# Optimization experiments

Hardware: AMD Instinct MI355X
Metric: run time of the kernel (lower is better)

## Reference

```python
import jax, jax.numpy as jnp
import numpy as np

TEMPERATURE = 0.07
N, D, NUM_CLASSES = 8192, 1024, 128


def setup_inputs() -> dict:
    key = jax.random.key(0)
    k1, k2 = jax.random.split(key)
    embeddings = jax.random.normal(k1, (N, D), dtype=jnp.float32)
    labels = jax.random.randint(k2, (N,), 0, NUM_CLASSES, dtype=jnp.int64)
    return {"embeddings": embeddings, "labels": labels}


def reference(embeddings, labels):
    # L2-normalize rows (eps matches F.normalize default clamp of 1e-12 on the norm)
    norm = jnp.maximum(jnp.linalg.norm(embeddings, axis=-1, keepdims=True), 1e-12)
    emb = embeddings / norm
    # [N, N] similarity scaled by temperature
    sim = jnp.matmul(emb, emb.T) / TEMPERATURE
    # positive mask: same label, diagonal zeroed
    pos_mask = (labels[:, None] == labels[None, :]).astype(sim.dtype)
    pos_mask = pos_mask * (1.0 - jnp.eye(sim.shape[0], dtype=sim.dtype))
    exp_sim = jnp.exp(sim)
    sum_exp = exp_sim.sum(axis=1)              # [N]
    pos_sum = (exp_sim * pos_mask).sum(axis=1)  # [N]
    loss = -jnp.log(pos_sum / sum_exp)
    return loss.mean()
```

## Files before the change

### kernel.cpp

```cpp
#include <hip/hip_runtime.h>
#include <hip/hip_bf16.h>
#include <math.h>

#define N 8192
#define D 1024
#define BM 256
#define BK 64
#define NTIL 32
#define NBLK 528
#define ITERS 8

typedef __bf16 bf16_t;
typedef bf16_t bf16x4 __attribute__((ext_vector_type(4)));
typedef bf16_t bf16x8 __attribute__((ext_vector_type(8)));
typedef float f32x4 __attribute__((ext_vector_type(4)));

__global__ __launch_bounds__(256) void norm_cast(const float* __restrict__ in,
                                                 bf16_t* __restrict__ out) {
    const int row = blockIdx.x;
    const int tid = threadIdx.x;
    const float4 v = ((const float4*)(in + (size_t)row * D))[tid];
    float ss = v.x * v.x + v.y * v.y + v.z * v.z + v.w * v.w;
    #pragma unroll
    for (int off = 32; off >= 1; off >>= 1) ss += __shfl_xor(ss, off, 64);
    __shared__ float red[4];
    const int wave = tid >> 6, lane = tid & 63;
    if (lane == 0) red[wave] = ss;
    __syncthreads();
    const float tot = red[0] + red[1] + red[2] + red[3];
    const float scale = 1.0f / fmaxf(sqrtf(tot), 1e-12f);
    bf16x4 o;
    o[0] = (bf16_t)(v.x * scale);
    o[1] = (bf16_t)(v.y * scale);
    o[2] = (bf16_t)(v.z * scale);
    o[3] = (bf16_t)(v.w * scale);
    ((bf16x4*)(out + (size_t)row * D))[tid] = o;
}

__global__ __launch_bounds__(512, 2) void gemm_fused(const bf16_t* __restrict__ E,
                                                     const int* __restrict__ labels,
                                                     float* __restrict__ sumExp,
                                                     float* __restrict__ posSum) {
    __shared__ bf16_t As[2][2][128 * 64];
    __shared__ bf16_t Bs[2][2][128 * 64];

    const int b0 = blockIdx.x;
    const int b  = (b0 & 7) * (NBLK / 8) + (b0 >> 3);

    int ti = (int)((sqrtf(8.0f * (float)b + 1.0f) - 1.0f) * 0.5f);
    while ((ti + 1) * (ti + 2) / 2 <= b) ++ti;
    while (ti * (ti + 1) / 2 > b) --ti;
    const int tj = b - ti * (ti + 1) / 2;
    const bool isDiag = (ti == tj);

    const int tid  = threadIdx.x;
    const int wave = tid >> 6;
    const int lane = tid & 63;
    const int lr   = lane & 15;
    const int q    = lane >> 4;
    const int wm   = wave >> 2;
    const int wn   = wave & 3;
    const int rowStart = ti * BM;
    const int colStart = tj * BM;

    f32x4 acc[8][4];
    #pragma unroll
    for (int m = 0; m < 8; ++m)
        #pragma unroll
        for (int n = 0; n < 4; ++n) acc[m][n] = {0.f, 0.f, 0.f, 0.f};

    const int r0  = tid >> 3;
    const int lu0 = (tid & 7) ^ (r0 & 7);
    const char* gA = (const char*)(E + (size_t)rowStart * D) + (size_t)r0 * (D * 2) + lu0 * 16;
    const char* gB = (const char*)(E + (size_t)colStart * D) + (size_t)r0 * (D * 2) + lu0 * 16;

    #define STAGE_A(buf, h, kb) do {                                                     \
        const char* g0_ = gA + (size_t)(h) * (128 * 2048) + (kb);                        \
        char* l0_ = (char*)&As[buf][h][0] + wave * 1024;                                 \
        __builtin_amdgcn_global_load_lds((const __attribute__((address_space(1))) void*)g0_, \
            (__attribute__((address_space(3))) void*)l0_, 16, 0, 0);                     \
        __builtin_amdgcn_global_load_lds(                                                \
            (const __attribute__((address_space(1))) void*)(g0_ + 64 * 2048),            \
            (__attribute__((address_space(3))) void*)(l0_ + 8192), 16, 0, 0);            \
    } while (0)
    #define STAGE_B(buf, h, kb) do {                                                     \
        const char* g0_ = gB + (size_t)(h) * (128 * 2048) + (kb);                        \
        char* l0_ = (char*)&Bs[buf][h][0] + wave * 1024;                                 \
        __builtin_amdgcn_global_load_lds((const __attribute__((address_space(1))) void*)g0_, \
            (__attribute__((address_space(3))) void*)l0_, 16, 0, 0);                     \
        __builtin_amdgcn_global_load_lds(                                                \
            (const __attribute__((address_space(1))) void*)(g0_ + 64 * 2048),            \
            (__attribute__((address_space(3))) void*)(l0_ + 8192), 16, 0, 0);            \
    } while (0)

    const int su0 = ((0 + q) ^ (lane & 7)) * 16;
    const int su1 = ((4 + q) ^ (lane & 7)) * 16;
    const char* rA0 = (const char*)&As[0][wm][0] + lr * 128;
    const char* rA1 = (const char*)&As[1][wm][0] + lr * 128;
    const char* rB0 = (const char*)&Bs[0][wn >> 1][0] + (wn & 1) * 8192 + lr * 128;
    const char* rB1 = (const char*)&Bs[1][wn >> 1][0] + (wn & 1) * 8192 + lr * 128;

    #define LD_A4(DST, RBASE, MOFFB, SU) do {                                            \
        _Pragma("unroll")                                                                \
        for (int m_ = 0; m_ < 4; ++m_)                                                   \
            DST[m_] = *(const bf16x8*)((RBASE) + (MOFFB) + m_ * 2048 + (SU));            \
    } while (0)
    #define LD_B4(DST, RBASE, SU) do {                                                   \
        _Pragma("unroll")                                                                \
        for (int n_ = 0; n_ < 4; ++n_)                                                   \
            DST[n_] = *(const bf16x8*)((RBASE) + n_ * 2048 + (SU));                      \
    } while (0)
    #define MFMA_QUAD(AF, BF, MO) do {                                                   \
        _Pragma("unroll")                                                                \
        for (int m_ = 0; m_ < 4; ++m_) {                                                 \
            _Pragma("unroll")                                                            \
            for (int n_ = 0; n_ < 4; ++n_)                                               \
                acc[(MO) + m_][n_] = __builtin_amdgcn_mfma_f32_16x16x32_bf16(            \
                    AF[m_], BF[n_], acc[(MO) + m_][n_], 0, 0, 0);                        \
        }                                                                                \
    } while (0)
    #define PHASE_MID() do {                                                             \
        __builtin_amdgcn_s_barrier();                                                    \
        asm volatile("s_waitcnt lgkmcnt(0)");                                            \
        __builtin_amdgcn_sched_barrier(0);                                               \
        __builtin_amdgcn_s_setprio(1);                                                   \
    } while (0)
    #define PHASE_END() do {                                                             \
        __builtin_amdgcn_s_setprio(0);                                                   \
        __builtin_amdgcn_s_barrier();                                                    \
    } while (0)

    bf16x8 a0[4], a1[4], bq0[4], bq1[4];

    STAGE_B(0, 0, 0);  STAGE_B(0, 1, 0);
    STAGE_A(0, 0, 0);  STAGE_A(0, 1, 0);
    STAGE_B(1, 0, 128); STAGE_B(1, 1, 128);
    asm volatile("s_waitcnt vmcnt(4)" ::: "memory");
    __builtin_amdgcn_sched_barrier(0);
    __builtin_amdgcn_s_barrier();

    #pragma unroll 1
    for (int it = 0; it < ITERS; ++it) {
        const bool lastIt = (it == ITERS - 1);
        const int kb1 = (2 * it + 1) * 128;
        const int kb2 = (2 * it + 2) * 128;
        const int kb3 = (2 * it + 3) * 128;

        LD_A4(a0, rA0, 0, su0);
        LD_B4(bq0, rB0, su0);
        STAGE_A(1, 0, kb1);
        PHASE_MID();
        MFMA_QUAD(a0, bq0, 0);
        PHASE_END();

        LD_A4(a1, rA0, 0, su1);
        LD_B4(bq1, rB0, su1);
        STAGE_A(1, 1, kb1);
        PHASE_MID();
        MFMA_QUAD(a1, bq1, 0);
        PHASE_END();

        LD_A4(a0, rA0, 8192, su0);
        if (!lastIt) STAGE_B(0, 0, kb2);
        PHASE_MID();
        MFMA_QUAD(a0, bq0, 4);
        PHASE_END();

        LD_A4(a1, rA0, 8192, su1);
        if (!lastIt) {
            STAGE_B(0, 1, kb2);
            asm volatile("s_waitcnt vmcnt(4)" ::: "memory");
        } else {
            asm volatile("s_waitcnt vmcnt(0)" ::: "memory");
        }
        __builtin_amdgcn_sched_barrier(0);
        PHASE_MID();
        MFMA_QUAD(a1, bq1, 4);
        PHASE_END();

        LD_A4(a0, rA1, 0, su0);
        LD_B4(bq0, rB1, su0);
        if (!lastIt) STAGE_A(0, 0, kb2);
        PHASE_MID();
        MFMA_QUAD(a0, bq0, 0);
        PHASE_END();

        LD_A4(a1, rA1, 0, su1);
        LD_B4(bq1, rB1, su1);
        if (!lastIt) STAGE_A(0, 1, kb2);
        PHASE_MID();
        MFMA_QUAD(a1, bq1, 0);
        PHASE_END();

        LD_A4(a0, rA1, 8192, su0);
        if (!lastIt) STAGE_B(1, 0, kb3);
        PHASE_MID();
        MFMA_QUAD(a0, bq0, 4);
        PHASE_END();

        LD_A4(a1, rA1, 8192, su1);
        if (!lastIt) {
            STAGE_B(1, 1, kb3);
            asm volatile("s_waitcnt vmcnt(4)" ::: "memory");
            __builtin_amdgcn_sched_barrier(0);
        }
        PHASE_MID();
        MFMA_QUAD(a1, bq1, 4);
        PHASE_END();
    }

    const float invT = 1.0f / 0.07f;
    int lc[4];
    #pragma unroll
    for (int n = 0; n < 4; ++n)
        lc[n] = labels[colStart + wn * 64 + n * 16 + lr];

    float colAll[4] = {0.f, 0.f, 0.f, 0.f};
    float colPos[4] = {0.f, 0.f, 0.f, 0.f};
    #pragma unroll
    for (int m = 0; m < 8; ++m) {
        #pragma unroll
        for (int e = 0; e < 4; ++e) {
            const int rloc = wm * 128 + m * 16 + q * 4 + e;
            const int gi   = rowStart + rloc;
            const int li   = labels[gi];
            float s_all = 0.f, s_pos = 0.f;
            #pragma unroll
            for (int n = 0; n < 4; ++n) {
                const int cloc = wn * 64 + n * 16 + lr;
                const int gj   = colStart + cloc;
                const float v  = __expf(acc[m][n][e] * invT);
                const bool same = (lc[n] == li);
                s_all += v;
                if (same && gi != gj) s_pos += v;
                if (!isDiag) {
                    colAll[n] += v;
                    if (same) colPos[n] += v;
                }
            }
            #pragma unroll
            for (int off = 1; off < 16; off <<= 1) {
                s_all += __shfl_xor(s_all, off, 64);
                s_pos += __shfl_xor(s_pos, off, 64);
            }
            if (lr == 0) {
                atomicAdd(&sumExp[gi], s_all);
                atomicAdd(&posSum[gi], s_pos);
            }
        }
    }
    if (!isDiag) {
        #pragma unroll
        for (int n = 0; n < 4; ++n) {
            float a = colAll[n], p = colPos[n];
            a += __shfl_xor(a, 16, 64);  a += __shfl_xor(a, 32, 64);
            p += __shfl_xor(p, 16, 64);  p += __shfl_xor(p, 32, 64);
            if (q == 0) {
                const int gj = colStart + wn * 64 + n * 16 + lr;
                atomicAdd(&sumExp[gj], a);
                atomicAdd(&posSum[gj], p);
            }
        }
    }
}

__global__ __launch_bounds__(1024) void finalize(const float* __restrict__ sumExp,
                                                 const float* __restrict__ posSum,
                                                 float* __restrict__ out) {
    const int tid = threadIdx.x;
    float s = 0.f;
    #pragma unroll
    for (int i = tid; i < N; i += 1024)
        s += __logf(sumExp[i] / posSum[i]);
    #pragma unroll
    for (int off = 32; off >= 1; off >>= 1) s += __shfl_xor(s, off, 64);
    __shared__ float red[16];
    if ((tid & 63) == 0) red[tid >> 6] = s;
    __syncthreads();
    if (tid == 0) {
        float t = 0.f;
        #pragma unroll
        for (int i = 0; i < 16; ++i) t += red[i];
        out[0] = t / (float)N;
    }
}

extern "C" void kernel_launch(void* const* d_in, const int* in_sizes, int n_in,
                              void* d_out, int out_size, void* d_ws, size_t ws_size,
                              hipStream_t stream) {
    const float* emb    = (const float*)d_in[0];
    const int*   labels = (const int*)d_in[1];
    float* out = (float*)d_out;

    float*  sumExp = (float*)d_ws;
    float*  posSum = sumExp + N;
    bf16_t* EN     = (bf16_t*)((char*)d_ws + (size_t)2 * N * sizeof(float));

    hipMemsetAsync(d_ws, 0, (size_t)2 * N * sizeof(float), stream);

    norm_cast<<<N, 256, 0, stream>>>(emb, EN);

    gemm_fused<<<NBLK, 512, 0, stream>>>(EN, labels, sumExp, posSum);

    finalize<<<1, 1024, 0, stream>>>(sumExp, posSum, out);
}
```

Baseline: 219.2 us.

## Double GEMM block to 16 waves with 64x64 per-wave tiles and fold memset

Each 256x256 tile is now computed by 1024 threads (16 waves), each owning a 64x64 sub-tile instead of 128x64. Global-to-LDS staging issues one load per thread, and the wait counts are lowered to match. The separate hipMemsetAsync is removed; norm_cast now zeroes the row accumulators. The point is more latency hiding and one fewer launch, paid for with lower register-level reuse (more LDS reads per MFMA). The tighter launch bound (1024,4) may also force register spilling.

After: 277.0 us. 1.26x slower.

```diff
diff --git a/kernel.cpp b/kernel.cpp
--- a/kernel.cpp
+++ b/kernel.cpp
@@ -16,9 +16,12 @@
 typedef float f32x4 __attribute__((ext_vector_type(4)));
 
 __global__ __launch_bounds__(256) void norm_cast(const float* __restrict__ in,
-                                                 bf16_t* __restrict__ out) {
+                                                 bf16_t* __restrict__ out,
+                                                 float* __restrict__ sumExp,
+                                                 float* __restrict__ posSum) {
     const int row = blockIdx.x;
     const int tid = threadIdx.x;
+    if (tid == 0) { sumExp[row] = 0.f; posSum[row] = 0.f; }
     const float4 v = ((const float4*)(in + (size_t)row * D))[tid];
     float ss = v.x * v.x + v.y * v.y + v.z * v.z + v.w * v.w;
     #pragma unroll
@@ -37,10 +40,10 @@
     ((bf16x4*)(out + (size_t)row * D))[tid] = o;
 }
 
-__global__ __launch_bounds__(512, 2) void gemm_fused(const bf16_t* __restrict__ E,
-                                                     const int* __restrict__ labels,
-                                                     float* __restrict__ sumExp,
-                                                     float* __restrict__ posSum) {
+__global__ __launch_bounds__(1024, 4) void gemm_fused(const bf16_t* __restrict__ E,
+                                                      const int* __restrict__ labels,
+                                                      float* __restrict__ sumExp,
+                                                      float* __restrict__ posSum) {
     __shared__ bf16_t As[2][2][128 * 64];
     __shared__ bf16_t Bs[2][2][128 * 64];
 
@@ -63,9 +66,9 @@
     const int rowStart = ti * BM;
     const int colStart = tj * BM;
 
-    f32x4 acc[8][4];
-    #pragma unroll
-    for (int m = 0; m < 8; ++m)
+    f32x4 acc[4][4];
+    #pragma unroll
+    for (int m = 0; m < 4; ++m)
         #pragma unroll
         for (int n = 0; n < 4; ++n) acc[m][n] = {0.f, 0.f, 0.f, 0.f};
 
@@ -75,48 +78,37 @@
     const char* gB = (const char*)(E + (size_t)colStart * D) + (size_t)r0 * (D * 2) + lu0 * 16;
 
     #define STAGE_A(buf, h, kb) do {                                                     \
-        const char* g0_ = gA + (size_t)(h) * (128 * 2048) + (kb);                        \
-        char* l0_ = (char*)&As[buf][h][0] + wave * 1024;                                 \
-        __builtin_amdgcn_global_load_lds((const __attribute__((address_space(1))) void*)g0_, \
-            (__attribute__((address_space(3))) void*)l0_, 16, 0, 0);                     \
-        __builtin_amdgcn_global_load_lds(                                                \
-            (const __attribute__((address_space(1))) void*)(g0_ + 64 * 2048),            \
-            (__attribute__((address_space(3))) void*)(l0_ + 8192), 16, 0, 0);            \
+        const char* g_ = gA + (size_t)(h) * (128 * 2048) + (kb);                         \
+        char* l_ = (char*)&As[buf][h][0] + wave * 1024;                                  \
+        __builtin_amdgcn_global_load_lds((const __attribute__((address_space(1))) void*)g_, \
+            (__attribute__((address_space(3))) void*)l_, 16, 0, 0);                      \
     } while (0)
     #define STAGE_B(buf, h, kb) do {                                                     \
-        const char* g0_ = gB + (size_t)(h) * (128 * 2048) + (kb);                        \
-        char* l0_ = (char*)&Bs[buf][h][0] + wave * 1024;                                 \
-        __builtin_amdgcn_global_load_lds((const __attribute__((address_space(1))) void*)g0_, \
-            (__attribute__((address_space(3))) void*)l0_, 16, 0, 0);                     \
-        __builtin_amdgcn_global_load_lds(                                                \
-            (const __attribute__((address_space(1))) void*)(g0_ + 64 * 2048),            \
-            (__attribute__((address_space(3))) void*)(l0_ + 8192), 16, 0, 0);            \
+        const char* g_ = gB + (size_t)(h) * (128 * 2048) + (kb);                         \
+        char* l_ = (char*)&Bs[buf][h][0] + wave * 1024;                                  \
+        __builtin_amdgcn_global_load_lds((const __attribute__((address_space(1))) void*)g_, \
+            (__attribute__((address_space(3))) void*)l_, 16, 0, 0);                      \
     } while (0)
 
     const int su0 = ((0 + q) ^ (lane & 7)) * 16;
     const int su1 = ((4 + q) ^ (lane & 7)) * 16;
-    const char* rA0 = (const char*)&As[0][wm][0] + lr * 128;
-    const char* rA1 = (const char*)&As[1][wm][0] + lr * 128;
-    const char* rB0 = (const char*)&Bs[0][wn >> 1][0] + (wn & 1) * 8192 + lr * 128;
-    const char* rB1 = (const char*)&Bs[1][wn >> 1][0] + (wn & 1) * 8192 + lr * 128;
-
-    #define LD_A4(DST, RBASE, MOFFB, SU) do {                                            \
+    const char* rA0 = (const char*)&As[0][wm >> 1][0] + ((wm & 1) * 64 + lr) * 128;
+    const char* rA1 = (const char*)&As[1][wm >> 1][0] + ((wm & 1) * 64 + lr) * 128;
+    const char* rB0 = (const char*)&Bs[0][wn >> 1][0] + ((wn & 1) * 64 + lr) * 128;
+    const char* rB1 = (const char*)&Bs[1][wn >> 1][0] + ((wn & 1) * 64 + lr) * 128;
+
+    #define LD4(DST, RBASE, SU) do {                                                     \
         _Pragma("unroll")                                                                \
-        for (int m_ = 0; m_ < 4; ++m_)                                                   \
-            DST[m_] = *(const bf16x8*)((RBASE) + (MOFFB) + m_ * 2048 + (SU));            \
-    } while (0)
-    #define LD_B4(DST, RBASE, SU) do {                                                   \
-        _Pragma("unroll")                                                                \
-        for (int n_ = 0; n_ < 4; ++n_)                                                   \
-            DST[n_] = *(const bf16x8*)((RBASE) + n_ * 2048 + (SU));                      \
-    } while (0)
-    #define MFMA_QUAD(AF, BF, MO) do {                                                   \
+        for (int i_ = 0; i_ < 4; ++i_)                                                   \
+            DST[i_] = *(const bf16x8*)((RBASE) + i_ * 2048 + (SU));                      \
+    } while (0)
+    #define MFMA8(AF, BF, NB) do {                                                       \
         _Pragma("unroll")                                                                \
         for (int m_ = 0; m_ < 4; ++m_) {                                                 \
             _Pragma("unroll")                                                            \
-            for (int n_ = 0; n_ < 4; ++n_)                                               \
-                acc[(MO) + m_][n_] = __builtin_amdgcn_mfma_f32_16x16x32_bf16(            \
-                    AF[m_], BF[n_], acc[(MO) + m_][n_], 0, 0, 0);                        \
+            for (int n_ = 0; n_ < 2; ++n_)                                               \
+                acc[m_][(NB) + n_] = __builtin_amdgcn_mfma_f32_16x16x32_bf16(            \
+                    AF[m_], BF[(NB) + n_], acc[m_][(NB) + n_], 0, 0, 0);                 \
         }                                                                                \
     } while (0)
     #define PHASE_MID() do {                                                             \
@@ -130,12 +122,12 @@
         __builtin_amdgcn_s_barrier();                                                    \
     } while (0)
 
-    bf16x8 a0[4], a1[4], bq0[4], bq1[4];
+    bf16x8 af[4], bf0[4], bf1[4];
 
     STAGE_B(0, 0, 0);  STAGE_B(0, 1, 0);
     STAGE_A(0, 0, 0);  STAGE_A(0, 1, 0);
     STAGE_B(1, 0, 128); STAGE_B(1, 1, 128);
-    asm volatile("s_waitcnt vmcnt(4)" ::: "memory");
+    asm volatile("s_waitcnt vmcnt(2)" ::: "memory");
     __builtin_amdgcn_sched_barrier(0);
     __builtin_amdgcn_s_barrier();
 
@@ -146,66 +138,62 @@
         const int kb2 = (2 * it + 2) * 128;
         const int kb3 = (2 * it + 3) * 128;
 
-        LD_A4(a0, rA0, 0, su0);
-        LD_B4(bq0, rB0, su0);
+        LD4(af,  rA0, su0);
+        LD4(bf0, rB0, su0);
         STAGE_A(1, 0, kb1);
         PHASE_MID();
-        MFMA_QUAD(a0, bq0, 0);
-        PHASE_END();
-
-        LD_A4(a1, rA0, 0, su1);
-        LD_B4(bq1, rB0, su1);
+        MFMA8(af, bf0, 0);
+        PHASE_END();
+
+        LD4(bf1, rB0, su1);
         STAGE_A(1, 1, kb1);
         PHASE_MID();
-        MFMA_QUAD(a1, bq1, 0);
-        PHASE_END();
-
-        LD_A4(a0, rA0, 8192, su0);
+        MFMA8(af, bf0, 2);
+        PHASE_END();
+
+        LD4(af, rA0, su1);
         if (!lastIt) STAGE_B(0, 0, kb2);
         PHASE_MID();
-        MFMA_QUAD(a0, bq0, 4);
-        PHASE_END();
-
-        LD_A4(a1, rA0, 8192, su1);
+        MFMA8(af, bf1, 0);
+        PHASE_END();
+
         if (!lastIt) {
             STAGE_B(0, 1, kb2);
-            asm volatile("s_waitcnt vmcnt(4)" ::: "memory");
+            asm volatile("s_waitcnt vmcnt(2)" ::: "memory");
         } else {
             asm volatile("s_waitcnt vmcnt(0)" ::: "memory");
         }
         __builtin_amdgcn_sched_barrier(0);
         PHASE_MID();
-        MFMA_QUAD(a1, bq1, 4);
-        PHASE_END();
-
-        LD_A4(a0, rA1, 0, su0);
-        LD_B4(bq0, rB1, su0);
+        MFMA8(af, bf1, 2);
+        PHASE_END();
+
+        LD4(af,  rA1, su0);
+        LD4(bf0, rB1, su0);
         if (!lastIt) STAGE_A(0, 0, kb2);
         PHASE_MID();
-        MFMA_QUAD(a0, bq0, 0);
-        PHASE_END();
-
-        LD_A4(a1, rA1, 0, su1);
-        LD_B4(bq1, rB1, su1);
+        MFMA8(af, bf0, 0);
+        PHASE_END();
+
+        LD4(bf1, rB1, su1);
         if (!lastIt) STAGE_A(0, 1, kb2);
         PHASE_MID();
-        MFMA_QUAD(a1, bq1, 0);
-        PHASE_END();
-
-        LD_A4(a0, rA1, 8192, su0);
+        MFMA8(af, bf0, 2);
+        PHASE_END();
+
+        LD4(af, rA1, su1);
         if (!lastIt) STAGE_B(1, 0, kb3);
         PHASE_MID();
-        MFMA_QUAD(a0, bq0, 4);
-        PHASE_END();
-
-        LD_A4(a1, rA1, 8192, su1);
+        MFMA8(af, bf1, 0);
+        PHASE_END();
+
         if (!lastIt) {
             STAGE_B(1, 1, kb3);
-            asm volatile("s_waitcnt vmcnt(4)" ::: "memory");
+            asm volatile("s_waitcnt vmcnt(2)" ::: "memory");
             __builtin_amdgcn_sched_barrier(0);
         }
         PHASE_MID();
-        MFMA_QUAD(a1, bq1, 4);
+        MFMA8(af, bf1, 2);
         PHASE_END();
     }
 
@@ -218,10 +206,10 @@
     float colAll[4] = {0.f, 0.f, 0.f, 0.f};
     float colPos[4] = {0.f, 0.f, 0.f, 0.f};
     #pragma unroll
-    for (int m = 0; m < 8; ++m) {
+    for (int m = 0; m < 4; ++m) {
         #pragma unroll
         for (int e = 0; e < 4; ++e) {
-            const int rloc = wm * 128 + m * 16 + q * 4 + e;
+            const int rloc = wm * 64 + m * 16 + q * 4 + e;
             const int gi   = rowStart + rloc;
             const int li   = labels[gi];
             float s_all = 0.f, s_pos = 0.f;
@@ -296,11 +284,9 @@
     float*  posSum = sumExp + N;
     bf16_t* EN     = (bf16_t*)((char*)d_ws + (size_t)2 * N * sizeof(float));
 
-    hipMemsetAsync(d_ws, 0, (size_t)2 * N * sizeof(float), stream);
-
-    norm_cast<<<N, 256, 0, stream>>>(emb, EN);
-
-    gemm_fused<<<NBLK, 512, 0, stream>>>(EN, labels, sumExp, posSum);
+    norm_cast<<<N, 256, 0, stream>>>(emb, EN, sumExp, posSum);
+
+    gemm_fused<<<NBLK, 1024, 0, stream>>>(EN, labels, sumExp, posSum);
 
     finalize<<<1, 1024, 0, stream>>>(sumExp, posSum, out);
 }
```
